# Optimization experiments

Measured on AMD Instinct MI355X. Metric: run time of the kernel, lower is better.

Reference implementation:

```python
import jax, jax.numpy as jnp
import numpy as np

B, S, E, H = 2, 2048, 1024, 16
D = E // H  # head_dim

def setup_inputs() -> dict:
    key = jax.random.key(0)
    k1, k2, k3 = jax.random.split(key, 3)
    x = jax.random.normal(k1, (B, S, E), dtype=jnp.float32)
    # xavier-uniform-ish scale for the learned projections
    lim_qkv = np.sqrt(6.0 / (E + 3 * E)).astype(np.float32)
    lim_out = np.sqrt(6.0 / (E + E)).astype(np.float32)
    w_qkv = jax.random.uniform(k2, (E, 3 * E), jnp.float32, -lim_qkv, lim_qkv)
    w_out = jax.random.uniform(k3, (E, E), jnp.float32, -lim_out, lim_out)
    return {"x": x, "w_qkv": w_qkv, "w_out": w_out}

def reference(x, w_qkv, w_out):
    b, s, e = x.shape
    # QKV projection: (B,S,E) @ (E,3E) -> (B,S,3E)
    qkv = jnp.einsum('bse,ef->bsf', x, w_qkv)
    qkv = qkv.reshape(b, s, 3, H, D).transpose(2, 0, 3, 1, 4)  # (3,B,H,S,D)
    q, k, v = qkv[0], qkv[1], qkv[2]
    scale = 1.0 / np.sqrt(D).astype(np.float32)
    scores = jnp.einsum('bhsd,bhtd->bhst', q, k) * scale  # (B,H,S,S)
    attn = jax.nn.softmax(scores, axis=-1)
    out = jnp.einsum('bhst,bhtd->bhsd', attn, v)  # (B,H,S,D)
    out = out.transpose(0, 2, 1, 3).reshape(b, s, e)
    return jnp.einsum('bse,ef->bsf', out, w_out)
```

## Files before the change

### kernel.cpp

```cpp
#include <hip/hip_runtime.h>
#include <cstdint>


typedef __bf16 bf16;
typedef __bf16 bf16x4 __attribute__((ext_vector_type(4)));
typedef __bf16 bf16x8 __attribute__((ext_vector_type(8)));
typedef float floatx4 __attribute__((ext_vector_type(4)));
typedef uint32_t u32;

#define B_ 2
#define S_ 2048
#define E_ 1024
#define H_ 16
#define D_ 64

__device__ __forceinline__ void async16(const void* g, const void* l) {
  __builtin_amdgcn_global_load_lds(
      (u32 __attribute__((address_space(1)))*)g,
      (u32 __attribute__((address_space(3)))*)l,
      16, 0, 0);
}

__device__ __forceinline__ void trans_tile(
    bf16* __restrict__ dst, const float* __restrict__ src, int R, int C,
    int c0, int r0, float (*t)[33]) {
  const int tx = threadIdx.x & 31, ty = threadIdx.x >> 5;
#pragma unroll
  for (int j = 0; j < 4; ++j)
    t[ty + 8 * j][tx] = src[(size_t)(r0 + ty + 8 * j) * C + c0 + tx];
  __syncthreads();
#pragma unroll
  for (int j = 0; j < 4; ++j)
    dst[(size_t)(c0 + ty + 8 * j) * R + r0 + tx] = (bf16)t[tx][ty + 8 * j];
}

__global__ __launch_bounds__(256) void prep(
    bf16* __restrict__ xb, bf16* __restrict__ wqkvT, bf16* __restrict__ woutT,
    const float* __restrict__ x, const float* __restrict__ wqkv,
    const float* __restrict__ wout) {
  __shared__ float t[32][33];
  const int id = blockIdx.x;
  if (id < 3072) {
    trans_tile(wqkvT, wqkv, 1024, 3072, (id % 96) * 32, (id / 96) * 32, t);
  } else if (id < 4096) {
    const int i2 = id - 3072;
    trans_tile(woutT, wout, 1024, 1024, (i2 % 32) * 32, (i2 / 32) * 32, t);
  } else {
    const int i = (id - 4096) * 256 + threadIdx.x;
    floatx4 v = ((const floatx4*)x)[i];
    bf16x4 o;
#pragma unroll
    for (int e = 0; e < 4; ++e) o[e] = (bf16)v[e];
    ((bf16x4*)xb)[i] = o;
  }
}

__global__ __launch_bounds__(256) void gemm_qkv(
    bf16* __restrict__ qb, bf16* __restrict__ kst, bf16* __restrict__ vst,
    const bf16* __restrict__ A, const bf16* __restrict__ Bt) {
  const int K_ = 1024;
  __shared__ alignas(16) bf16 sA[3][4096];
  __shared__ alignas(16) bf16 sB[3][4096];
  const int tid = threadIdx.x;
  const int lane = tid & 63;
  const int w = tid >> 6;
  const int wr = (w >> 1) * 64, wc = (w & 1) * 64;
  const int l15 = lane & 15, l4 = lane >> 4;
  const int m0 = blockIdx.x * 128;
  const int n0 = blockIdx.y * 128;

  const bf16* ga0 = A + (size_t)(m0 + lane) * K_ + w * 8;
  const bf16* gb0 = Bt + (size_t)(n0 + lane) * K_ + w * 8;
  const int da0 = (w * 128 + lane) * 8;

  floatx4 acc[4][4];
#pragma unroll
  for (int i = 0; i < 4; ++i)
#pragma unroll
    for (int j = 0; j < 4; ++j) acc[i][j] = (floatx4){0.f, 0.f, 0.f, 0.f};

#pragma unroll
  for (int g = 0; g < 2; ++g) {
    async16(ga0 + (size_t)g * 64 * K_, &sA[0][da0 + g * 64 * 8]);
    async16(gb0 + (size_t)g * 64 * K_, &sB[0][da0 + g * 64 * 8]);
  }
#pragma unroll
  for (int g = 0; g < 2; ++g) {
    async16(ga0 + (size_t)g * 64 * K_ + 32, &sA[1][da0 + g * 64 * 8]);
    async16(gb0 + (size_t)g * 64 * K_ + 32, &sB[1][da0 + g * 64 * 8]);
  }
  asm volatile("s_waitcnt vmcnt(4)" ::: "memory");
  asm volatile("s_barrier" ::: "memory");

  int cur = 0, stb = 2;
  for (int t = 0; t < 32; ++t) {
    if (t < 30) {
      const int k0 = (t + 2) * 32;
#pragma unroll
      for (int g = 0; g < 2; ++g) {
        async16(ga0 + (size_t)g * 64 * K_ + k0, &sA[stb][da0 + g * 64 * 8]);
        async16(gb0 + (size_t)g * 64 * K_ + k0, &sB[stb][da0 + g * 64 * 8]);
      }
    }

    bf16x8 af[4], bfr[4];
#pragma unroll
    for (int i = 0; i < 4; ++i)
      af[i] = *(const bf16x8*)&sA[cur][(l4 * 128 + wr + i * 16 + l15) * 8];
#pragma unroll
    for (int j = 0; j < 4; ++j)
      bfr[j] = *(const bf16x8*)&sB[cur][(l4 * 128 + wc + j * 16 + l15) * 8];

    __builtin_amdgcn_s_setprio(1);
#pragma unroll
    for (int i = 0; i < 4; ++i)
#pragma unroll
      for (int j = 0; j < 4; ++j)
        acc[i][j] = __builtin_amdgcn_mfma_f32_16x16x32_bf16(af[i], bfr[j],
                                                            acc[i][j], 0, 0, 0);
    __builtin_amdgcn_s_setprio(0);

    if (t < 30)
      asm volatile("s_waitcnt vmcnt(4)" ::: "memory");
    else
      asm volatile("s_waitcnt vmcnt(0)" ::: "memory");
    asm volatile("s_barrier" ::: "memory");

    cur = (cur == 2) ? 0 : cur + 1;
    stb = (stb == 2) ? 0 : stb + 1;
  }

  if (n0 < E_) {
#pragma unroll
    for (int i = 0; i < 4; ++i)
#pragma unroll
      for (int j = 0; j < 4; ++j)
#pragma unroll
        for (int r = 0; r < 4; ++r) {
          const int row = m0 + wr + i * 16 + l4 * 4 + r;
          const int col = n0 + wc + j * 16 + l15;
          qb[(size_t)row * E_ + col] = (bf16)acc[i][j][r];
        }
  } else if (n0 < 2 * E_) {
#pragma unroll
    for (int i = 0; i < 4; ++i)
#pragma unroll
      for (int j = 0; j < 4; ++j) {
        const int f = n0 - E_ + wc + j * 16 + l15;
        const int h = f >> 6, d = f & 63;
        const int kg = d >> 3, jd = d & 7;
        const int row0 = m0 + wr + i * 16 + l4 * 4;
        const int b = row0 >> 11, s0 = row0 & 2047;
        const int tt = s0 >> 6, key0 = s0 & 63;
        const size_t base =
            ((((size_t)(b * H_ + h) * 32 + tt) * 8 + kg) * 64 + key0) * 8 + jd;
#pragma unroll
        for (int r = 0; r < 4; ++r)
          kst[base + (size_t)r * 8] = (bf16)acc[i][j][r];
      }
  } else {
#pragma unroll
    for (int i = 0; i < 4; ++i)
#pragma unroll
      for (int j = 0; j < 4; ++j) {
        const int f = n0 - 2 * E_ + wc + j * 16 + l15;
        const int h = f >> 6, d = f & 63;
        const int row0 = m0 + wr + i * 16 + l4 * 4;
        const int b = row0 >> 11, s0 = row0 & 2047;
        const int tt = s0 >> 6, k6 = s0 & 63;
        const int kg = (k6 >> 5) * 4 + ((k6 >> 2) & 3);
        const int e0 = ((k6 >> 4) & 1) * 4;
        bf16x4 o;
#pragma unroll
        for (int r = 0; r < 4; ++r) o[r] = (bf16)acc[i][j][r];
        *(bf16x4*)(vst +
                   ((((size_t)(b * H_ + h) * 32 + tt) * 8 + kg) * 64 + d) * 8 +
                   e0) = o;
      }
  }
}

template <typename OutT>
__global__ __launch_bounds__(256) void gemm_bt64(
    OutT* __restrict__ C, const bf16* __restrict__ A, const bf16* __restrict__ Bt,
    int M, int N, int K) {
  __shared__ alignas(16) bf16 sA[3][2048];
  __shared__ alignas(16) bf16 sB[3][4096];
  const int tid = threadIdx.x;
  const int lane = tid & 63;
  const int w = tid >> 6;
  const int wr = (w >> 1) * 32, wc = (w & 1) * 64;
  const int l15 = lane & 15, l4 = lane >> 4;
  const int m0 = blockIdx.x * 64;
  const int n0 = blockIdx.y * 128;

  const bf16* ga0 = A + (size_t)(m0 + lane) * K + w * 8;
  const bf16* gb0 = Bt + (size_t)(n0 + lane) * K + w * 8;
  const int daA = (w * 64 + lane) * 8;
  const int daB = (w * 128 + lane) * 8;

  floatx4 acc[2][4];
#pragma unroll
  for (int i = 0; i < 2; ++i)
#pragma unroll
    for (int j = 0; j < 4; ++j) acc[i][j] = (floatx4){0.f, 0.f, 0.f, 0.f};

#pragma unroll
  for (int tb = 0; tb < 2; ++tb) {
    async16(ga0 + tb * 32, &sA[tb][daA]);
#pragma unroll
    for (int g = 0; g < 2; ++g)
      async16(gb0 + (size_t)g * 64 * K + tb * 32, &sB[tb][daB + g * 64 * 8]);
  }
  asm volatile("s_waitcnt vmcnt(3)" ::: "memory");
  asm volatile("s_barrier" ::: "memory");

  int cur = 0, stb = 2;
  const int NT = K / 32;
  for (int t = 0; t < NT; ++t) {
    if (t < NT - 2) {
      const int k0 = (t + 2) * 32;
      async16(ga0 + k0, &sA[stb][daA]);
#pragma unroll
      for (int g = 0; g < 2; ++g)
        async16(gb0 + (size_t)g * 64 * K + k0, &sB[stb][daB + g * 64 * 8]);
    }

    bf16x8 af[2], bfr[4];
#pragma unroll
    for (int i = 0; i < 2; ++i)
      af[i] = *(const bf16x8*)&sA[cur][(l4 * 64 + wr + i * 16 + l15) * 8];
#pragma unroll
    for (int j = 0; j < 4; ++j)
      bfr[j] = *(const bf16x8*)&sB[cur][(l4 * 128 + wc + j * 16 + l15) * 8];

    __builtin_amdgcn_s_setprio(1);
#pragma unroll
    for (int i = 0; i < 2; ++i)
#pragma unroll
      for (int j = 0; j < 4; ++j)
        acc[i][j] = __builtin_amdgcn_mfma_f32_16x16x32_bf16(af[i], bfr[j],
                                                            acc[i][j], 0, 0, 0);
    __builtin_amdgcn_s_setprio(0);

    if (t < NT - 2)
      asm volatile("s_waitcnt vmcnt(3)" ::: "memory");
    else
      asm volatile("s_waitcnt vmcnt(0)" ::: "memory");
    asm volatile("s_barrier" ::: "memory");

    cur = (cur == 2) ? 0 : cur + 1;
    stb = (stb == 2) ? 0 : stb + 1;
  }

#pragma unroll
  for (int i = 0; i < 2; ++i)
#pragma unroll
    for (int j = 0; j < 4; ++j)
#pragma unroll
      for (int r = 0; r < 4; ++r) {
        const int row = m0 + wr + i * 16 + l4 * 4 + r;
        const int col = n0 + wc + j * 16 + l15;
        C[(size_t)row * N + col] = (OutT)acc[i][j][r];
      }
}

__global__ __launch_bounds__(256) void attn_flash(
    bf16* __restrict__ attn, const bf16* __restrict__ qb,
    const bf16* __restrict__ kst, const bf16* __restrict__ vst) {
  __shared__ alignas(16) bf16 sK[2][4096];
  __shared__ alignas(16) bf16 sV[2][4096];
  const int tid = threadIdx.x;
  const int lane = tid & 63;
  const int w = tid >> 6;
  const int l15 = lane & 15, l4 = lane >> 4;
  const int bh = blockIdx.x;
  const int q0 = blockIdx.y * 64;
  const int b = bh >> 4, h = bh & 15;
  const bf16* kb = kst + (size_t)bh * (S_ * D_);
  const bf16* vb = vst + (size_t)bh * (S_ * D_);

  bf16x8 qf[2];
#pragma unroll
  for (int ks = 0; ks < 2; ++ks) {
    bf16x8 t = *(const bf16x8*)(qb +
        (size_t)(b * S_ + q0 + w * 16 + l15) * E_ + h * D_ + ks * 32 + l4 * 8);
#pragma unroll
    for (int e = 0; e < 8; ++e)
      t[e] = (bf16)((float)t[e] * 0.180336878f);
    qf[ks] = t;
  }

  floatx4 O[4];
#pragma unroll
  for (int j = 0; j < 4; ++j) O[j] = (floatx4){0.f, 0.f, 0.f, 0.f};
  float l_s = 0.f;

#pragma unroll
  for (int j = 0; j < 2; ++j) {
    const int kg = w * 2 + j;
    async16(kb + (size_t)(kg * 64 + lane) * 8, &sK[0][(kg * 64 + lane) * 8]);
    async16(vb + (size_t)(kg * 64 + lane) * 8, &sV[0][(kg * 64 + lane) * 8]);
  }

  for (int t = 0; t < 32; ++t) {
    const int cur = t & 1, nxt = cur ^ 1;
    __syncthreads();

    if (t < 31) {
#pragma unroll
      for (int j = 0; j < 2; ++j) {
        const int kg = w * 2 + j;
        const size_t goff = ((size_t)((t + 1) * 8 + kg) * 64 + lane) * 8;
        async16(kb + goff, &sK[nxt][(kg * 64 + lane) * 8]);
        async16(vb + goff, &sV[nxt][(kg * 64 + lane) * 8]);
      }
    }

    floatx4 sc[4];
#pragma unroll
    for (int j = 0; j < 4; ++j) sc[j] = (floatx4){-16.f, -16.f, -16.f, -16.f};
#pragma unroll
    for (int ks = 0; ks < 2; ++ks) {
      bf16x8 kf[4];
#pragma unroll
      for (int kt = 0; kt < 4; ++kt)
        kf[kt] = *(const bf16x8*)&sK[cur][((ks * 4 + l4) * 64 + kt * 16 + l15) * 8];
#pragma unroll
      for (int kt = 0; kt < 4; ++kt)
        sc[kt] = __builtin_amdgcn_mfma_f32_16x16x32_bf16(
            kf[kt], qf[ks], sc[kt], 0, 0, 0);
    }

    float rs = 0.f;
    bf16x8 pf[2];
#pragma unroll
    for (int kt = 0; kt < 4; ++kt) {
#pragma unroll
      for (int r = 0; r < 4; ++r) {
        const float p = __builtin_amdgcn_exp2f(sc[kt][r]);
        rs += p;
        pf[kt >> 1][(kt & 1) * 4 + r] = (bf16)p;
      }
    }
    l_s += rs;

#pragma unroll
    for (int ks = 0; ks < 2; ++ks) {
      bf16x8 vf[4];
#pragma unroll
      for (int dt = 0; dt < 4; ++dt)
        vf[dt] = *(const bf16x8*)&sV[cur][((ks * 4 + l4) * 64 + dt * 16 + l15) * 8];
#pragma unroll
      for (int dt = 0; dt < 4; ++dt)
        O[dt] = __builtin_amdgcn_mfma_f32_16x16x32_bf16(vf[dt], pf[ks], O[dt], 0, 0, 0);
    }
  }

  float l = l_s;
  l += __shfl_xor(l, 16);
  l += __shfl_xor(l, 32);
  const float inv_l = 1.f / l;
  const int row = q0 + w * 16 + l15;
#pragma unroll
  for (int dt = 0; dt < 4; ++dt) {
    bf16x4 o;
#pragma unroll
    for (int r = 0; r < 4; ++r) o[r] = (bf16)(O[dt][r] * inv_l);
    *(bf16x4*)(attn + ((size_t)b * S_ + row) * E_ + h * D_ + dt * 16 + l4 * 4) = o;
  }
}

extern "C" void kernel_launch(void* const* d_in, const int* in_sizes, int n_in,
                              void* d_out, int out_size, void* d_ws, size_t ws_size,
                              hipStream_t stream) {
  const float* x = (const float*)d_in[0];
  const float* wqkv = (const float*)d_in[1];
  const float* wout = (const float*)d_in[2];
  float* out = (float*)d_out;

  bf16* ws = (bf16*)d_ws;
  bf16* xb = ws;
  bf16* qb = xb + (size_t)4096 * 1024;
  bf16* wqkvT = qb + (size_t)4096 * 1024;
  bf16* woutT = wqkvT + (size_t)3072 * 1024;
  bf16* kst = woutT + (size_t)1024 * 1024;
  bf16* vst = kst + (size_t)B_ * H_ * S_ * D_;
  bf16* attn = vst + (size_t)B_ * H_ * S_ * D_;

  prep<<<dim3(8192), 256, 0, stream>>>(xb, wqkvT, woutT, x, wqkv, wout);
  gemm_qkv<<<dim3(32, 24), 256, 0, stream>>>(qb, kst, vst, xb, wqkvT);
  attn_flash<<<dim3(B_ * H_, S_ / 64), 256, 0, stream>>>(attn, qb, kst, vst);
  gemm_bt64<float><<<dim3(64, 8), 256, 0, stream>>>(out, attn, woutT, 4096, E_, E_);
}
```

Before: 209.7 us.

## Pre-tile GEMM operands into contiguous LDS-ready blocks for linear async loads

Measured after the change: 177.7 us. 1.18x faster.

```diff
diff --git a/kernel.cpp b/kernel.cpp
--- a/kernel.cpp
+++ b/kernel.cpp
@@ -21,44 +21,50 @@
       16, 0, 0);
 }
 
-__device__ __forceinline__ void trans_tile(
-    bf16* __restrict__ dst, const float* __restrict__ src, int R, int C,
-    int c0, int r0, float (*t)[33]) {
-  const int tx = threadIdx.x & 31, ty = threadIdx.x >> 5;
-#pragma unroll
-  for (int j = 0; j < 4; ++j)
-    t[ty + 8 * j][tx] = src[(size_t)(r0 + ty + 8 * j) * C + c0 + tx];
-  __syncthreads();
-#pragma unroll
-  for (int j = 0; j < 4; ++j)
-    dst[(size_t)(c0 + ty + 8 * j) * R + r0 + tx] = (bf16)t[tx][ty + 8 * j];
-}
-
 __global__ __launch_bounds__(256) void prep(
-    bf16* __restrict__ xb, bf16* __restrict__ wqkvT, bf16* __restrict__ woutT,
+    bf16* __restrict__ xt, bf16* __restrict__ wqt, bf16* __restrict__ wot,
     const float* __restrict__ x, const float* __restrict__ wqkv,
     const float* __restrict__ wout) {
-  __shared__ float t[32][33];
   const int id = blockIdx.x;
-  if (id < 3072) {
-    trans_tile(wqkvT, wqkv, 1024, 3072, (id % 96) * 32, (id / 96) * 32, t);
-  } else if (id < 4096) {
-    const int i2 = id - 3072;
-    trans_tile(woutT, wout, 1024, 1024, (i2 % 32) * 32, (i2 / 32) * 32, t);
+  const int tid = threadIdx.x;
+  if (id < 1024) {
+    const bf16 isW = (id < 768);
+    const int i2 = isW ? id : id - 768;
+    const int nblk = i2 >> 5, t = i2 & 31;
+    const float* src = isW ? wqkv : wout;
+    bf16* dst = isW ? wqt : wot;
+    const int C = isW ? 3072 : 1024;
+#pragma unroll
+    for (int p = 0; p < 2; ++p) {
+      const int u = p * 256 + tid;
+      const int kg = u >> 7, row = u & 127;
+      const float* s = src + (size_t)(t * 32 + kg * 8) * C + nblk * 128 + row;
+      bf16x8 o;
+#pragma unroll
+      for (int j = 0; j < 8; ++j) o[j] = (bf16)s[(size_t)j * C];
+      *(bf16x8*)(dst + ((((size_t)nblk * 32 + t) * 4 + kg) * 128 + row) * 8) = o;
+    }
   } else {
-    const int i = (id - 4096) * 256 + threadIdx.x;
-    floatx4 v = ((const floatx4*)x)[i];
-    bf16x4 o;
-#pragma unroll
-    for (int e = 0; e < 4; ++e) o[e] = (bf16)v[e];
-    ((bf16x4*)xb)[i] = o;
+    const int i3 = id - 1024;
+    const int mblk = i3 >> 5, t = i3 & 31;
+#pragma unroll
+    for (int p = 0; p < 2; ++p) {
+      const int u = p * 256 + tid;
+      const int kg = u >> 7, row = u & 127;
+      const floatx4* s = (const floatx4*)(
+          x + (size_t)(mblk * 128 + row) * 1024 + t * 32 + kg * 8);
+      floatx4 v0 = s[0], v1 = s[1];
+      bf16x8 o;
+#pragma unroll
+      for (int j = 0; j < 4; ++j) { o[j] = (bf16)v0[j]; o[4 + j] = (bf16)v1[j]; }
+      *(bf16x8*)(xt + ((((size_t)mblk * 32 + t) * 4 + kg) * 128 + row) * 8) = o;
+    }
   }
 }
 
 __global__ __launch_bounds__(256) void gemm_qkv(
     bf16* __restrict__ qb, bf16* __restrict__ kst, bf16* __restrict__ vst,
-    const bf16* __restrict__ A, const bf16* __restrict__ Bt) {
-  const int K_ = 1024;
+    const bf16* __restrict__ At, const bf16* __restrict__ Bt) {
   __shared__ alignas(16) bf16 sA[3][4096];
   __shared__ alignas(16) bf16 sB[3][4096];
   const int tid = threadIdx.x;
@@ -69,8 +75,8 @@
   const int m0 = blockIdx.x * 128;
   const int n0 = blockIdx.y * 128;
 
-  const bf16* ga0 = A + (size_t)(m0 + lane) * K_ + w * 8;
-  const bf16* gb0 = Bt + (size_t)(n0 + lane) * K_ + w * 8;
+  const bf16* ga0 = At + (size_t)blockIdx.x * 131072 + (w * 128 + lane) * 8;
+  const bf16* gb0 = Bt + (size_t)blockIdx.y * 131072 + (w * 128 + lane) * 8;
   const int da0 = (w * 128 + lane) * 8;
 
   floatx4 acc[4][4];
@@ -80,26 +86,23 @@
     for (int j = 0; j < 4; ++j) acc[i][j] = (floatx4){0.f, 0.f, 0.f, 0.f};
 
 #pragma unroll
-  for (int g = 0; g < 2; ++g) {
-    async16(ga0 + (size_t)g * 64 * K_, &sA[0][da0 + g * 64 * 8]);
-    async16(gb0 + (size_t)g * 64 * K_, &sB[0][da0 + g * 64 * 8]);
-  }
-#pragma unroll
-  for (int g = 0; g < 2; ++g) {
-    async16(ga0 + (size_t)g * 64 * K_ + 32, &sA[1][da0 + g * 64 * 8]);
-    async16(gb0 + (size_t)g * 64 * K_ + 32, &sB[1][da0 + g * 64 * 8]);
-  }
+  for (int tb = 0; tb < 2; ++tb)
+#pragma unroll
+    for (int g = 0; g < 2; ++g) {
+      async16(ga0 + (size_t)tb * 4096 + g * 512, &sA[tb][da0 + g * 512]);
+      async16(gb0 + (size_t)tb * 4096 + g * 512, &sB[tb][da0 + g * 512]);
+    }
   asm volatile("s_waitcnt vmcnt(4)" ::: "memory");
   asm volatile("s_barrier" ::: "memory");
 
   int cur = 0, stb = 2;
   for (int t = 0; t < 32; ++t) {
     if (t < 30) {
-      const int k0 = (t + 2) * 32;
+      const size_t k0 = (size_t)(t + 2) * 4096;
 #pragma unroll
       for (int g = 0; g < 2; ++g) {
-        async16(ga0 + (size_t)g * 64 * K_ + k0, &sA[stb][da0 + g * 64 * 8]);
-        async16(gb0 + (size_t)g * 64 * K_ + k0, &sB[stb][da0 + g * 64 * 8]);
+        async16(ga0 + k0 + g * 512, &sA[stb][da0 + g * 512]);
+        async16(gb0 + k0 + g * 512, &sB[stb][da0 + g * 512]);
       }
     }
 
@@ -182,7 +185,7 @@
 
 template <typename OutT>
 __global__ __launch_bounds__(256) void gemm_bt64(
-    OutT* __restrict__ C, const bf16* __restrict__ A, const bf16* __restrict__ Bt,
+    OutT* __restrict__ C, const bf16* __restrict__ At, const bf16* __restrict__ Bt,
     int M, int N, int K) {
   __shared__ alignas(16) bf16 sA[3][2048];
   __shared__ alignas(16) bf16 sB[3][4096];
@@ -194,8 +197,8 @@
   const int m0 = blockIdx.x * 64;
   const int n0 = blockIdx.y * 128;
 
-  const bf16* ga0 = A + (size_t)(m0 + lane) * K + w * 8;
-  const bf16* gb0 = Bt + (size_t)(n0 + lane) * K + w * 8;
+  const bf16* ga0 = At + (size_t)blockIdx.x * (K * 64) + (w * 64 + lane) * 8;
+  const bf16* gb0 = Bt + (size_t)blockIdx.y * (K * 128) + (w * 128 + lane) * 8;
   const int daA = (w * 64 + lane) * 8;
   const int daB = (w * 128 + lane) * 8;
 
@@ -207,10 +210,10 @@
 
 #pragma unroll
   for (int tb = 0; tb < 2; ++tb) {
-    async16(ga0 + tb * 32, &sA[tb][daA]);
+    async16(ga0 + (size_t)tb * 2048, &sA[tb][daA]);
 #pragma unroll
     for (int g = 0; g < 2; ++g)
-      async16(gb0 + (size_t)g * 64 * K + tb * 32, &sB[tb][daB + g * 64 * 8]);
+      async16(gb0 + (size_t)tb * 4096 + g * 512, &sB[tb][daB + g * 512]);
   }
   asm volatile("s_waitcnt vmcnt(3)" ::: "memory");
   asm volatile("s_barrier" ::: "memory");
@@ -219,11 +222,10 @@
   const int NT = K / 32;
   for (int t = 0; t < NT; ++t) {
     if (t < NT - 2) {
-      const int k0 = (t + 2) * 32;
-      async16(ga0 + k0, &sA[stb][daA]);
+      async16(ga0 + (size_t)(t + 2) * 2048, &sA[stb][daA]);
 #pragma unroll
       for (int g = 0; g < 2; ++g)
-        async16(gb0 + (size_t)g * 64 * K + k0, &sB[stb][daB + g * 64 * 8]);
+        async16(gb0 + (size_t)(t + 2) * 4096 + g * 512, &sB[stb][daB + g * 512]);
     }
 
     bf16x8 af[2], bfr[4];
@@ -266,7 +268,7 @@
 }
 
 __global__ __launch_bounds__(256) void attn_flash(
-    bf16* __restrict__ attn, const bf16* __restrict__ qb,
+    bf16* __restrict__ at, const bf16* __restrict__ qb,
     const bf16* __restrict__ kst, const bf16* __restrict__ vst) {
   __shared__ alignas(16) bf16 sK[2][4096];
   __shared__ alignas(16) bf16 sV[2][4096];
@@ -361,13 +363,18 @@
   l += __shfl_xor(l, 16);
   l += __shfl_xor(l, 32);
   const float inv_l = 1.f / l;
-  const int row = q0 + w * 16 + l15;
+  const int mblk = b * 32 + blockIdx.y;
+  const int row6 = w * 16 + l15;
 #pragma unroll
   for (int dt = 0; dt < 4; ++dt) {
     bf16x4 o;
 #pragma unroll
     for (int r = 0; r < 4; ++r) o[r] = (bf16)(O[dt][r] * inv_l);
-    *(bf16x4*)(attn + ((size_t)b * S_ + row) * E_ + h * D_ + dt * 16 + l4 * 4) = o;
+    const int tt = h * 2 + (dt >> 1);
+    const int kg = (dt & 1) * 2 + (l4 >> 1);
+    const int jd = (l4 & 1) * 4;
+    *(bf16x4*)(at +
+               ((((size_t)mblk * 32 + tt) * 4 + kg) * 64 + row6) * 8 + jd) = o;
   }
 }
 
@@ -380,16 +387,16 @@
   float* out = (float*)d_out;
 
   bf16* ws = (bf16*)d_ws;
-  bf16* xb = ws;
-  bf16* qb = xb + (size_t)4096 * 1024;
-  bf16* wqkvT = qb + (size_t)4096 * 1024;
-  bf16* woutT = wqkvT + (size_t)3072 * 1024;
-  bf16* kst = woutT + (size_t)1024 * 1024;
+  bf16* xt = ws;
+  bf16* qb = xt + (size_t)4096 * 1024;
+  bf16* wqt = qb + (size_t)4096 * 1024;
+  bf16* wot = wqt + (size_t)3072 * 1024;
+  bf16* kst = wot + (size_t)1024 * 1024;
   bf16* vst = kst + (size_t)B_ * H_ * S_ * D_;
-  bf16* attn = vst + (size_t)B_ * H_ * S_ * D_;
-
-  prep<<<dim3(8192), 256, 0, stream>>>(xb, wqkvT, woutT, x, wqkv, wout);
-  gemm_qkv<<<dim3(32, 24), 256, 0, stream>>>(qb, kst, vst, xb, wqkvT);
-  attn_flash<<<dim3(B_ * H_, S_ / 64), 256, 0, stream>>>(attn, qb, kst, vst);
-  gemm_bt64<float><<<dim3(64, 8), 256, 0, stream>>>(out, attn, woutT, 4096, E_, E_);
-}
+  bf16* at = vst + (size_t)B_ * H_ * S_ * D_;
+
+  prep<<<dim3(2048), 256, 0, stream>>>(xt, wqt, wot, x, wqkv, wout);
+  gemm_qkv<<<dim3(32, 24), 256, 0, stream>>>(qb, kst, vst, xt, wqt);
+  attn_flash<<<dim3(B_ * H_, S_ / 64), 256, 0, stream>>>(at, qb, kst, vst);
+  gemm_bt64<float><<<dim3(64, 8), 256, 0, stream>>>(out, at, wot, 4096, E_, E_);
+}
```
